# Kernel optimization log

Measured on AMD Instinct MI355X. Metric: run time of the kernel, lower is better.

The kernel has to match this reference:

```python
import jax, jax.numpy as jnp
import numpy as np

N = 100000      # nodes
IN = 64         # in_channels
HID = 64        # hidden_channels
H2 = HID // 2   # per-sign channels
E = 1600000     # edges per sign


def _mean_aggr(x_src, edge_index, num_nodes):
    """Mean of x_src[src] scattered onto dst (PyG mean aggregation)."""
    src, dst = edge_index[0], edge_index[1]
    s = jax.ops.segment_sum(x_src[src], dst, num_segments=num_nodes)
    cnt = jax.ops.segment_sum(jnp.ones((src.shape[0],), x_src.dtype), dst,
                              num_segments=num_nodes)
    return s / jnp.maximum(cnt, 1.0)[:, None]


def setup_inputs() -> dict:
    key = jax.random.key(0)
    ks = jax.random.split(key, 12)
    x = jax.random.normal(ks[0], (N, IN), jnp.float32)
    pos_edge_index = jax.random.randint(ks[1], (2, E), 0, N)
    neg_edge_index = jax.random.randint(ks[2], (2, E), 0, N)

    def w(k, fan_in, fan_out):
        b = 1.0 / np.sqrt(fan_in)
        return jax.random.uniform(k, (fan_in, fan_out), jnp.float32, -b, b)

    return dict(
        x=x, pos_edge_index=pos_edge_index, neg_edge_index=neg_edge_index,
        # conv1 (first_aggr=True): lin_l (no bias applied via l), lin_r (bias)
        w1_pl=w(ks[3], IN, H2), w1_pr=w(ks[4], IN, H2), b1_p=jnp.zeros((H2,), jnp.float32),
        w1_nl=w(ks[5], IN, H2), w1_nr=w(ks[6], IN, H2), b1_n=jnp.zeros((H2,), jnp.float32),
        # conv2 (first_aggr=False): lin_l over cat of two aggregations (2*H2), lin_r over H2
        w2_pl=w(ks[7], 2 * H2, H2), w2_pr=w(ks[8], H2, H2), b2_p=jnp.zeros((H2,), jnp.float32),
        w2_nl=w(ks[9], 2 * H2, H2), w2_nr=w(ks[10], H2, H2), b2_n=jnp.zeros((H2,), jnp.float32),
    )


def reference(x, pos_edge_index, neg_edge_index,
              w1_pl, w1_pr, b1_p, w1_nl, w1_nr, b1_n,
              w2_pl, w2_pr, b2_p, w2_nl, w2_nr, b2_n):
    n = x.shape[0]
    # --- conv1, first_aggr=True ---
    agg_p = _mean_aggr(x, pos_edge_index, n)          # [N, IN]
    agg_n = _mean_aggr(x, neg_edge_index, n)
    out_pos = agg_p @ w1_pl + x @ w1_pr + b1_p         # [N, H2]
    out_neg = agg_n @ w1_nl + x @ w1_nr + b1_n
    z = jax.nn.relu(jnp.concatenate([out_pos, out_neg], axis=-1))  # [N, HID]

    # --- conv2, first_aggr=False ---
    h2 = z.shape[-1] // 2
    zp, zn = z[:, :h2], z[:, h2:]
    p1 = _mean_aggr(zp, pos_edge_index, n)
    p2 = _mean_aggr(zn, neg_edge_index, n)
    out_pos = jnp.concatenate([p1, p2], axis=-1) @ w2_pl + zp @ w2_pr + b2_p
    n1 = _mean_aggr(zn, pos_edge_index, n)
    n2 = _mean_aggr(zp, neg_edge_index, n)
    out_neg = jnp.concatenate([n1, n2], axis=-1) @ w2_nl + zn @ w2_nr + b2_n
    z = jax.nn.relu(jnp.concatenate([out_pos, out_neg], axis=-1))  # [N, HID]
    return z
```

## Files before the change

kernel.cpp:

```cpp
#include <hip/hip_runtime.h>
#include <hip/hip_fp16.h>

using uint = unsigned int;

static constexpr int NN  = 100000;
static constexpr int NE  = 1600000;
static constexpr int DIM = 64;
static constexpr int HH  = 32;
static constexpr int NBLK = (NN + 255) / 256;
static constexpr int HB   = 256;
static constexpr int CHUNK = NE / HB;
static constexpr int BSH  = 9;
static constexpr int BSZ  = 512;
static constexpr int NBKT = (NN + BSZ - 1) / BSZ;

__device__ __forceinline__ float2 up16(uint v) {
  __half2 h = *reinterpret_cast<__half2*>(&v);
  return __half22float2(h);
}
__device__ __forceinline__ uint pk16(float a, float b) {
  __half2 h = __floats2half2_rn(a, b);
  return *reinterpret_cast<uint*>(&h);
}


__global__ void c_hist(const int* __restrict__ pe, const int* __restrict__ ne,
                       int* __restrict__ part_hist) {
  const int set = blockIdx.y;
  const int* dstA = (set ? ne : pe) + NE;
  __shared__ int h[256];
  h[threadIdx.x] = 0;
  __syncthreads();
  int lo = blockIdx.x * CHUNK;
  int hi = lo + CHUNK;
  for (int i = lo + threadIdx.x; i < hi; i += 256)
    atomicAdd(&h[dstA[i] >> BSH], 1);
  __syncthreads();
  part_hist[(set * HB + blockIdx.x) * 256 + threadIdx.x] = h[threadIdx.x];
}

__global__ void c_colscan(int* __restrict__ part_hist, int* __restrict__ tot) {
  const int set = blockIdx.y;
  const int k   = blockIdx.x;
  const int t   = threadIdx.x;
  int v = part_hist[(set * HB + t) * 256 + k];
  __shared__ int sm[256];
  sm[t] = v;
  __syncthreads();
  for (int off = 1; off < 256; off <<= 1) {
    int add = (t >= off) ? sm[t - off] : 0;
    __syncthreads();
    sm[t] += add;
    __syncthreads();
  }
  part_hist[(set * HB + t) * 256 + k] = (t == 0) ? 0 : sm[t - 1];
  if (t == 255) tot[set * 256 + k] = sm[255];
}

__global__ void c_basescan(const int* __restrict__ tot, int* __restrict__ base) {
  const int t   = threadIdx.x;
  const int seg = t >> 8;
  const int idx = t & 255;
  int v = tot[seg * 256 + idx];
  __shared__ int sm[512];
  sm[t] = v;
  __syncthreads();
  for (int off = 1; off < 256; off <<= 1) {
    int add = (idx >= off) ? sm[t - off] : 0;
    __syncthreads();
    sm[t] += add;
    __syncthreads();
  }
  base[seg * 257 + idx] = (idx == 0) ? 0 : sm[t - 1];
  if (idx == 255) base[seg * 257 + 256] = sm[t];
}

__global__ void c_scatter(const int* __restrict__ pe, const int* __restrict__ ne,
                          const int* __restrict__ part_hist, const int* __restrict__ base,
                          int2* __restrict__ partP, int2* __restrict__ partN) {
  const int set = blockIdx.y;
  const int* srcA = set ? ne : pe;
  const int* dstA = srcA + NE;
  int2* part = set ? partN : partP;
  __shared__ int off[256];
  off[threadIdx.x] = base[set * 257 + threadIdx.x] +
                     part_hist[(set * HB + blockIdx.x) * 256 + threadIdx.x];
  __syncthreads();
  int lo = blockIdx.x * CHUNK;
  int hi = lo + CHUNK;
  for (int i = lo + threadIdx.x; i < hi; i += 256) {
    int src = srcA[i];
    int dst = dstA[i];
    int pos = atomicAdd(&off[dst >> BSH], 1);
    part[pos] = make_int2(src, dst);
  }
}

__global__ void c_bucket(const int2* __restrict__ partP, const int2* __restrict__ partN,
                         const int* __restrict__ base,
                         int* __restrict__ row_p, int* __restrict__ row_n,
                         int* __restrict__ col_p, int* __restrict__ col_n,
                         const float* __restrict__ x,
                         const float* __restrict__ w1_pl, const float* __restrict__ w1_pr,
                         const float* __restrict__ b1_p,
                         const float* __restrict__ w1_nl, const float* __restrict__ w1_nr,
                         const float* __restrict__ b1_n,
                         uint* __restrict__ y1u, float* __restrict__ r1) {
  const int bx = blockIdx.x;
  const int t  = threadIdx.x;

  if (bx < 2 * NBKT) {
    const int set = bx / NBKT;
    const int k   = bx - set * NBKT;
    const int2* part = set ? partN : partP;
    int* row = set ? row_n : row_p;
    int* col = set ? col_n : col_p;
    const int lo = k * BSZ;
    const int hi = min(lo + BSZ, NN);
    const int s = base[set * 257 + k];
    const int e = base[set * 257 + k + 1];

    __shared__ int cnt[BSZ], rowl[BSZ], cnt2[BSZ];
    cnt[t] = 0; cnt[t + 256] = 0;
    cnt2[t] = 0; cnt2[t + 256] = 0;
    __syncthreads();
    for (int i = s + t; i < e; i += 256)
      atomicAdd(&cnt[part[i].y - lo], 1);
    __syncthreads();
    rowl[t] = cnt[t]; rowl[t + 256] = cnt[t + 256];
    __syncthreads();
    for (int off = 1; off < BSZ; off <<= 1) {
      int a0 = (t >= off) ? rowl[t - off] : 0;
      int a1 = (t + 256 >= off) ? rowl[t + 256 - off] : 0;
      __syncthreads();
      rowl[t] += a0; rowl[t + 256] += a1;
      __syncthreads();
    }
    if (lo + t < hi)        row[lo + t]        = s + (t ? rowl[t - 1] : 0);
    if (lo + t + 256 < hi)  row[lo + t + 256]  = s + rowl[t + 255];
    if (k == NBKT - 1 && t == 0) row[NN] = NE;
    for (int i = s + t; i < e; i += 256) {
      int2 p = part[i];
      int l = p.y - lo;
      int pos = s + (l ? rowl[l - 1] : 0) + atomicAdd(&cnt2[l], 1);
      col[pos] = p.x;
    }
    return;
  }

  const int pb   = bx - 2 * NBKT;
  const int h    = (pb >= NBLK) ? 1 : 0;
  const int nblk = pb - (h ? NBLK : 0);
  const float* wl   = h ? w1_nl : w1_pl;
  const float* wr   = h ? w1_nr : w1_pr;
  const float* bias = h ? b1_n  : b1_p;

  __shared__ float s_wl[DIM][HH];
  __shared__ float s_wr[DIM][HH];
  for (int i = t; i < DIM * HH; i += 256) {
    s_wl[i >> 5][i & 31] = wl[i];
    s_wr[i >> 5][i & 31] = wr[i];
  }
  __syncthreads();

  int node = nblk * 256 + t;
  if (node >= NN) return;

  float ay[HH], ar[HH];
#pragma unroll
  for (int j = 0; j < HH; ++j) { ay[j] = 0.f; ar[j] = bias[j]; }

  const float4* xrow = (const float4*)(x + (size_t)node * DIM);
#pragma unroll 4
  for (int k4 = 0; k4 < DIM / 4; ++k4) {
    float4 xv = xrow[k4];
#pragma unroll
    for (int u = 0; u < 4; ++u) {
      int k = k4 * 4 + u;
      float xk = (&xv.x)[u];
#pragma unroll
      for (int j = 0; j < HH; ++j) {
        ay[j] += xk * s_wl[k][j];
        ar[j] += xk * s_wr[k][j];
      }
    }
  }

  uint*  yo = y1u + (size_t)node * 32 + h * 16;
  float* ro = r1  + (size_t)node * 64 + h * 32;
#pragma unroll
  for (int j = 0; j < 16; ++j) yo[j] = pk16(ay[2 * j], ay[2 * j + 1]);
#pragma unroll
  for (int j = 0; j < HH; ++j) ro[j] = ar[j];
}

__global__ void k_aggr1(const uint* __restrict__ y1u,
                        const int* __restrict__ rp, const int* __restrict__ cp,
                        const int* __restrict__ rn, const int* __restrict__ cn,
                        const float* r1,
                        float* z) {
  int gid  = blockIdx.x * 256 + threadIdx.x;
  int node = gid >> 6;
  if (node >= NN) return;
  int lane = threadIdx.x & 63;
  int g = lane >> 3;
  int f = lane & 7;

  int s = rp[node], e = rp[node + 1];
  float a0 = 0.f, a1 = 0.f, a2 = 0.f, a3 = 0.f;
  for (int i = s + g; i < e; i += 8) {
    int c = cp[i];
    uint2 v = *(const uint2*)&y1u[(size_t)c * 32 + 2 * f];
    float2 lo = up16(v.x), hi = up16(v.y);
    a0 += lo.x; a1 += lo.y; a2 += hi.x; a3 += hi.y;
  }
#pragma unroll
  for (int w = 8; w <= 32; w <<= 1) {
    a0 += __shfl_xor(a0, w); a1 += __shfl_xor(a1, w);
    a2 += __shfl_xor(a2, w); a3 += __shfl_xor(a3, w);
  }
  float invp = 1.f / (float)max(e - s, 1);

  s = rn[node]; e = rn[node + 1];
  float b0 = 0.f, b1 = 0.f, b2 = 0.f, b3 = 0.f;
  for (int i = s + g; i < e; i += 8) {
    int c = cn[i];
    uint2 v = *(const uint2*)&y1u[(size_t)c * 32 + 16 + 2 * f];
    float2 lo = up16(v.x), hi = up16(v.y);
    b0 += lo.x; b1 += lo.y; b2 += hi.x; b3 += hi.y;
  }
#pragma unroll
  for (int w = 8; w <= 32; w <<= 1) {
    b0 += __shfl_xor(b0, w); b1 += __shfl_xor(b1, w);
    b2 += __shfl_xor(b2, w); b3 += __shfl_xor(b3, w);
  }
  float invn = 1.f / (float)max(e - s, 1);

  size_t base = (size_t)node * 64;
  if (g == 0) {
    const float4 r = *(const float4*)(r1 + base + 4 * f);
    float4 o;
    o.x = fmaxf(a0 * invp + r.x, 0.f);
    o.y = fmaxf(a1 * invp + r.y, 0.f);
    o.z = fmaxf(a2 * invp + r.z, 0.f);
    o.w = fmaxf(a3 * invp + r.w, 0.f);
    *(float4*)(z + base + 4 * f) = o;
  } else if (g == 1) {
    const float4 r = *(const float4*)(r1 + base + 32 + 4 * f);
    float4 o;
    o.x = fmaxf(b0 * invn + r.x, 0.f);
    o.y = fmaxf(b1 * invn + r.y, 0.f);
    o.z = fmaxf(b2 * invn + r.z, 0.f);
    o.w = fmaxf(b3 * invn + r.w, 0.f);
    *(float4*)(z + base + 32 + 4 * f) = o;
  }
}

__global__ void k_mid(const float* __restrict__ z,
                      const float* __restrict__ w2_pl, const float* __restrict__ w2_pr,
                      const float* __restrict__ b2_p,
                      const float* __restrict__ w2_nl, const float* __restrict__ w2_nr,
                      const float* __restrict__ b2_n,
                      uint* __restrict__ u_pos, uint* __restrict__ u_neg,
                      float* __restrict__ r2) {
  const int t = blockIdx.y;
  const float* mat;
  const float* bias = nullptr;
  int srcHalf;
  switch (t) {
    case 0: mat = w2_pl;            srcHalf = 0; break;
    case 1: mat = w2_nl;            srcHalf = 1; break;
    case 2: mat = w2_pl + 32 * 32;  srcHalf = 1; break;
    case 3: mat = w2_nl + 32 * 32;  srcHalf = 0; break;
    case 4: mat = w2_pr; bias = b2_p; srcHalf = 0; break;
    default: mat = w2_nr; bias = b2_n; srcHalf = 1; break;
  }

  __shared__ float s_m[HH][HH];
  for (int i = threadIdx.x; i < HH * HH; i += 256) s_m[i >> 5][i & 31] = mat[i];
  __syncthreads();

  int node = blockIdx.x * 256 + threadIdx.x;
  if (node >= NN) return;

  float acc[HH];
#pragma unroll
  for (int j = 0; j < HH; ++j) acc[j] = bias ? bias[j] : 0.f;

  const float4* zrow = (const float4*)(z + (size_t)node * 64 + srcHalf * 32);
#pragma unroll 4
  for (int k4 = 0; k4 < HH / 4; ++k4) {
    float4 v = zrow[k4];
#pragma unroll
    for (int u = 0; u < 4; ++u) {
      int k = k4 * 4 + u;
      float vv = (&v.x)[u];
#pragma unroll
      for (int j = 0; j < HH; ++j) acc[j] += vv * s_m[k][j];
    }
  }

  if (t < 4) {
    uint* o = (t < 2 ? u_pos : u_neg) + (size_t)node * 32 + (t & 1) * 16;
#pragma unroll
    for (int j = 0; j < 16; ++j) o[j] = pk16(acc[2 * j], acc[2 * j + 1]);
  } else {
    float* o = r2 + (size_t)node * 64 + (t - 4) * 32;
#pragma unroll
    for (int j = 0; j < HH; ++j) o[j] = acc[j];
  }
}

__global__ void k_aggr2(const uint* __restrict__ u_pos, const uint* __restrict__ u_neg,
                        const int* __restrict__ rp, const int* __restrict__ cp,
                        const int* __restrict__ rn, const int* __restrict__ cn,
                        const float* __restrict__ r2,
                        float* __restrict__ out) {
  int gid  = blockIdx.x * 256 + threadIdx.x;
  int node = gid >> 6;
  if (node >= NN) return;
  int lane = threadIdx.x & 63;
  int g = lane >> 4;
  int f = lane & 15;

  int s = rp[node], e = rp[node + 1];
  float a0 = 0.f, a1 = 0.f, a2 = 0.f, a3 = 0.f;
  for (int i = s + g; i < e; i += 4) {
    int c = cp[i];
    uint2 v = *(const uint2*)&u_pos[(size_t)c * 32 + 2 * f];
    float2 lo = up16(v.x), hi = up16(v.y);
    a0 += lo.x; a1 += lo.y; a2 += hi.x; a3 += hi.y;
  }
#pragma unroll
  for (int w = 16; w <= 32; w <<= 1) {
    a0 += __shfl_xor(a0, w); a1 += __shfl_xor(a1, w);
    a2 += __shfl_xor(a2, w); a3 += __shfl_xor(a3, w);
  }
  float invp = 1.f / (float)max(e - s, 1);

  s = rn[node]; e = rn[node + 1];
  float b0 = 0.f, b1 = 0.f, b2 = 0.f, b3 = 0.f;
  for (int i = s + g; i < e; i += 4) {
    int c = cn[i];
    uint2 v = *(const uint2*)&u_neg[(size_t)c * 32 + 2 * f];
    float2 lo = up16(v.x), hi = up16(v.y);
    b0 += lo.x; b1 += lo.y; b2 += hi.x; b3 += hi.y;
  }
#pragma unroll
  for (int w = 16; w <= 32; w <<= 1) {
    b0 += __shfl_xor(b0, w); b1 += __shfl_xor(b1, w);
    b2 += __shfl_xor(b2, w); b3 += __shfl_xor(b3, w);
  }
  float invn = 1.f / (float)max(e - s, 1);

  if (g == 0) {
    size_t base = (size_t)node * 64 + 4 * f;
    const float4 r = *(const float4*)(r2 + base);
    float4 o;
    o.x = fmaxf(a0 * invp + b0 * invn + r.x, 0.f);
    o.y = fmaxf(a1 * invp + b1 * invn + r.y, 0.f);
    o.z = fmaxf(a2 * invp + b2 * invn + r.z, 0.f);
    o.w = fmaxf(a3 * invp + b3 * invn + r.w, 0.f);
    *(float4*)(out + base) = o;
  }
}


extern "C" void kernel_launch(void* const* d_in, const int* in_sizes, int n_in,
                              void* d_out, int out_size, void* d_ws, size_t ws_size,
                              hipStream_t stream) {
  const float* x     = (const float*)d_in[0];
  const int*   pe    = (const int*)d_in[1];
  const int*   ne    = (const int*)d_in[2];
  const float* w1_pl = (const float*)d_in[3];
  const float* w1_pr = (const float*)d_in[4];
  const float* b1_p  = (const float*)d_in[5];
  const float* w1_nl = (const float*)d_in[6];
  const float* w1_nr = (const float*)d_in[7];
  const float* b1_n  = (const float*)d_in[8];
  const float* w2_pl = (const float*)d_in[9];
  const float* w2_pr = (const float*)d_in[10];
  const float* b2_p  = (const float*)d_in[11];
  const float* w2_nl = (const float*)d_in[12];
  const float* w2_nr = (const float*)d_in[13];
  const float* b2_n  = (const float*)d_in[14];

  char* ws = (char*)d_ws;
  size_t off = 0;
  auto alloc = [&](size_t bytes) -> char* {
    char* p = ws + off;
    off = (off + bytes + 255) & ~(size_t)255;
    return p;
  };

  int* row_p = (int*)alloc((size_t)(NN + 1) * 4);
  int* row_n = (int*)alloc((size_t)(NN + 1) * 4);
  int* col_p = (int*)alloc((size_t)NE * 4);
  int* col_n = (int*)alloc((size_t)NE * 4);
  int* part_hist = (int*)alloc((size_t)2 * HB * 256 * 4);
  int* tot   = (int*)alloc((size_t)2 * 256 * 4);
  int* base  = (int*)alloc((size_t)2 * 257 * 4);

  char* regA  = alloc((size_t)2 * NE * 8);
  int2* partP = (int2*)regA;
  int2* partN = (int2*)(regA + (size_t)NE * 8);
  uint* u_pos = (uint*)regA;
  uint* u_neg = (uint*)(regA + (size_t)NN * 32 * 4);

  char*  regB = alloc((size_t)NN * 64 * 4);
  uint*  y1u  = (uint*)regB;
  float* r2   = (float*)regB;

  float* r1 = (float*)d_out;
  float* z  = (float*)d_out;

  const int nb = NBLK;
  const int ab = (NN * 64 + 255) / 256;

  dim3 hg(HB, 2);
  c_hist<<<hg, 256, 0, stream>>>(pe, ne, part_hist);
  dim3 cg(256, 2);
  c_colscan<<<cg, 256, 0, stream>>>(part_hist, tot);
  c_basescan<<<1, 512, 0, stream>>>(tot, base);
  c_scatter<<<hg, 256, 0, stream>>>(pe, ne, part_hist, base, partP, partN);
  c_bucket<<<2 * NBKT + 2 * NBLK, 256, 0, stream>>>(
      partP, partN, base, row_p, row_n, col_p, col_n,
      x, w1_pl, w1_pr, b1_p, w1_nl, w1_nr, b1_n, y1u, r1);

  k_aggr1<<<ab, 256, 0, stream>>>(y1u, row_p, col_p, row_n, col_n, r1, z);

  dim3 g2(nb, 6);
  k_mid<<<g2, 256, 0, stream>>>(z, w2_pl, w2_pr, b2_p, w2_nl, w2_nr, b2_n,
                                u_pos, u_neg, r2);

  k_aggr2<<<ab, 256, 0, stream>>>(u_pos, u_neg, row_p, col_p, row_n, col_n, r2,
                                  (float*)d_out);
}
```

Baseline: 318.5 us.

## Pack partition entries into one word and widen gather loads to 16 bytes

The partition buffer now stores each edge as a single 32-bit word, with the source shifted left and the bucket-local destination in the low 9 bits, replacing the int2 pair. This halves scatter and bucket-pass traffic and shrinks the workspace region. Both aggregation kernels now load 16 bytes per lane (8 halves) with more edge groups per node, which adds shuffle-reduction steps in exchange for fewer, wider gather loads. Packing relies on source indices fitting in 23 bits, which holds for the 100000 nodes.

```diff
diff --git a/kernel.cpp b/kernel.cpp
--- a/kernel.cpp
+++ b/kernel.cpp
@@ -77,11 +77,11 @@
 
 __global__ void c_scatter(const int* __restrict__ pe, const int* __restrict__ ne,
                           const int* __restrict__ part_hist, const int* __restrict__ base,
-                          int2* __restrict__ partP, int2* __restrict__ partN) {
+                          uint* __restrict__ partP, uint* __restrict__ partN) {
   const int set = blockIdx.y;
   const int* srcA = set ? ne : pe;
   const int* dstA = srcA + NE;
-  int2* part = set ? partN : partP;
+  uint* part = set ? partN : partP;
   __shared__ int off[256];
   off[threadIdx.x] = base[set * 257 + threadIdx.x] +
                      part_hist[(set * HB + blockIdx.x) * 256 + threadIdx.x];
@@ -92,11 +92,11 @@
     int src = srcA[i];
     int dst = dstA[i];
     int pos = atomicAdd(&off[dst >> BSH], 1);
-    part[pos] = make_int2(src, dst);
-  }
-}
-
-__global__ void c_bucket(const int2* __restrict__ partP, const int2* __restrict__ partN,
+    part[pos] = ((uint)src << BSH) | (uint)(dst & (BSZ - 1));
+  }
+}
+
+__global__ void c_bucket(const uint* __restrict__ partP, const uint* __restrict__ partN,
                          const int* __restrict__ base,
                          int* __restrict__ row_p, int* __restrict__ row_n,
                          int* __restrict__ col_p, int* __restrict__ col_n,
@@ -112,7 +112,7 @@
   if (bx < 2 * NBKT) {
     const int set = bx / NBKT;
     const int k   = bx - set * NBKT;
-    const int2* part = set ? partN : partP;
+    const uint* part = set ? partN : partP;
     int* row = set ? row_n : row_p;
     int* col = set ? col_n : col_p;
     const int lo = k * BSZ;
@@ -125,7 +125,7 @@
     cnt2[t] = 0; cnt2[t + 256] = 0;
     __syncthreads();
     for (int i = s + t; i < e; i += 256)
-      atomicAdd(&cnt[part[i].y - lo], 1);
+      atomicAdd(&cnt[part[i] & (BSZ - 1)], 1);
     __syncthreads();
     rowl[t] = cnt[t]; rowl[t + 256] = cnt[t + 256];
     __syncthreads();
@@ -140,10 +140,10 @@
     if (lo + t + 256 < hi)  row[lo + t + 256]  = s + rowl[t + 255];
     if (k == NBKT - 1 && t == 0) row[NN] = NE;
     for (int i = s + t; i < e; i += 256) {
-      int2 p = part[i];
-      int l = p.y - lo;
+      uint p = part[i];
+      int l = p & (BSZ - 1);
       int pos = s + (l ? rowl[l - 1] : 0) + atomicAdd(&cnt2[l], 1);
-      col[pos] = p.x;
+      col[pos] = (int)(p >> BSH);
     }
     return;
   }
@@ -203,56 +203,74 @@
   int node = gid >> 6;
   if (node >= NN) return;
   int lane = threadIdx.x & 63;
-  int g = lane >> 3;
-  int f = lane & 7;
+  int g = lane >> 2;
+  int f = lane & 3;
 
   int s = rp[node], e = rp[node + 1];
-  float a0 = 0.f, a1 = 0.f, a2 = 0.f, a3 = 0.f;
-  for (int i = s + g; i < e; i += 8) {
+  float a[8];
+#pragma unroll
+  for (int j = 0; j < 8; ++j) a[j] = 0.f;
+  for (int i = s + g; i < e; i += 16) {
     int c = cp[i];
-    uint2 v = *(const uint2*)&y1u[(size_t)c * 32 + 2 * f];
-    float2 lo = up16(v.x), hi = up16(v.y);
-    a0 += lo.x; a1 += lo.y; a2 += hi.x; a3 += hi.y;
-  }
-#pragma unroll
-  for (int w = 8; w <= 32; w <<= 1) {
-    a0 += __shfl_xor(a0, w); a1 += __shfl_xor(a1, w);
-    a2 += __shfl_xor(a2, w); a3 += __shfl_xor(a3, w);
+    uint4 v = *(const uint4*)&y1u[(size_t)c * 32 + 4 * f];
+    float2 p0 = up16(v.x), p1 = up16(v.y), p2 = up16(v.z), p3 = up16(v.w);
+    a[0] += p0.x; a[1] += p0.y; a[2] += p1.x; a[3] += p1.y;
+    a[4] += p2.x; a[5] += p2.y; a[6] += p3.x; a[7] += p3.y;
+  }
+#pragma unroll
+  for (int w = 4; w <= 32; w <<= 1) {
+#pragma unroll
+    for (int j = 0; j < 8; ++j) a[j] += __shfl_xor(a[j], w);
   }
   float invp = 1.f / (float)max(e - s, 1);
 
   s = rn[node]; e = rn[node + 1];
-  float b0 = 0.f, b1 = 0.f, b2 = 0.f, b3 = 0.f;
-  for (int i = s + g; i < e; i += 8) {
+  float b[8];
+#pragma unroll
+  for (int j = 0; j < 8; ++j) b[j] = 0.f;
+  for (int i = s + g; i < e; i += 16) {
     int c = cn[i];
-    uint2 v = *(const uint2*)&y1u[(size_t)c * 32 + 16 + 2 * f];
-    float2 lo = up16(v.x), hi = up16(v.y);
-    b0 += lo.x; b1 += lo.y; b2 += hi.x; b3 += hi.y;
-  }
-#pragma unroll
-  for (int w = 8; w <= 32; w <<= 1) {
-    b0 += __shfl_xor(b0, w); b1 += __shfl_xor(b1, w);
-    b2 += __shfl_xor(b2, w); b3 += __shfl_xor(b3, w);
+    uint4 v = *(const uint4*)&y1u[(size_t)c * 32 + 16 + 4 * f];
+    float2 p0 = up16(v.x), p1 = up16(v.y), p2 = up16(v.z), p3 = up16(v.w);
+    b[0] += p0.x; b[1] += p0.y; b[2] += p1.x; b[3] += p1.y;
+    b[4] += p2.x; b[5] += p2.y; b[6] += p3.x; b[7] += p3.y;
+  }
+#pragma unroll
+  for (int w = 4; w <= 32; w <<= 1) {
+#pragma unroll
+    for (int j = 0; j < 8; ++j) b[j] += __shfl_xor(b[j], w);
   }
   float invn = 1.f / (float)max(e - s, 1);
 
   size_t base = (size_t)node * 64;
   if (g == 0) {
-    const float4 r = *(const float4*)(r1 + base + 4 * f);
-    float4 o;
-    o.x = fmaxf(a0 * invp + r.x, 0.f);
-    o.y = fmaxf(a1 * invp + r.y, 0.f);
-    o.z = fmaxf(a2 * invp + r.z, 0.f);
-    o.w = fmaxf(a3 * invp + r.w, 0.f);
-    *(float4*)(z + base + 4 * f) = o;
+    const float4 r0 = *(const float4*)(r1 + base + 8 * f);
+    const float4 r1v = *(const float4*)(r1 + base + 8 * f + 4);
+    float4 o0, o1;
+    o0.x = fmaxf(a[0] * invp + r0.x, 0.f);
+    o0.y = fmaxf(a[1] * invp + r0.y, 0.f);
+    o0.z = fmaxf(a[2] * invp + r0.z, 0.f);
+    o0.w = fmaxf(a[3] * invp + r0.w, 0.f);
+    o1.x = fmaxf(a[4] * invp + r1v.x, 0.f);
+    o1.y = fmaxf(a[5] * invp + r1v.y, 0.f);
+    o1.z = fmaxf(a[6] * invp + r1v.z, 0.f);
+    o1.w = fmaxf(a[7] * invp + r1v.w, 0.f);
+    *(float4*)(z + base + 8 * f) = o0;
+    *(float4*)(z + base + 8 * f + 4) = o1;
   } else if (g == 1) {
-    const float4 r = *(const float4*)(r1 + base + 32 + 4 * f);
-    float4 o;
-    o.x = fmaxf(b0 * invn + r.x, 0.f);
-    o.y = fmaxf(b1 * invn + r.y, 0.f);
-    o.z = fmaxf(b2 * invn + r.z, 0.f);
-    o.w = fmaxf(b3 * invn + r.w, 0.f);
-    *(float4*)(z + base + 32 + 4 * f) = o;
+    const float4 r0 = *(const float4*)(r1 + base + 32 + 8 * f);
+    const float4 r1v = *(const float4*)(r1 + base + 32 + 8 * f + 4);
+    float4 o0, o1;
+    o0.x = fmaxf(b[0] * invn + r0.x, 0.f);
+    o0.y = fmaxf(b[1] * invn + r0.y, 0.f);
+    o0.z = fmaxf(b[2] * invn + r0.z, 0.f);
+    o0.w = fmaxf(b[3] * invn + r0.w, 0.f);
+    o1.x = fmaxf(b[4] * invn + r1v.x, 0.f);
+    o1.y = fmaxf(b[5] * invn + r1v.y, 0.f);
+    o1.z = fmaxf(b[6] * invn + r1v.z, 0.f);
+    o1.w = fmaxf(b[7] * invn + r1v.w, 0.f);
+    *(float4*)(z + base + 32 + 8 * f) = o0;
+    *(float4*)(z + base + 32 + 8 * f + 4) = o1;
   }
 }
 
@@ -320,48 +338,60 @@
   int node = gid >> 6;
   if (node >= NN) return;
   int lane = threadIdx.x & 63;
-  int g = lane >> 4;
-  int f = lane & 15;
+  int g = lane >> 3;
+  int f = lane & 7;
 
   int s = rp[node], e = rp[node + 1];
-  float a0 = 0.f, a1 = 0.f, a2 = 0.f, a3 = 0.f;
-  for (int i = s + g; i < e; i += 4) {
+  float a[8];
+#pragma unroll
+  for (int j = 0; j < 8; ++j) a[j] = 0.f;
+  for (int i = s + g; i < e; i += 8) {
     int c = cp[i];
-    uint2 v = *(const uint2*)&u_pos[(size_t)c * 32 + 2 * f];
-    float2 lo = up16(v.x), hi = up16(v.y);
-    a0 += lo.x; a1 += lo.y; a2 += hi.x; a3 += hi.y;
-  }
-#pragma unroll
-  for (int w = 16; w <= 32; w <<= 1) {
-    a0 += __shfl_xor(a0, w); a1 += __shfl_xor(a1, w);
-    a2 += __shfl_xor(a2, w); a3 += __shfl_xor(a3, w);
+    uint4 v = *(const uint4*)&u_pos[(size_t)c * 32 + 4 * f];
+    float2 p0 = up16(v.x), p1 = up16(v.y), p2 = up16(v.z), p3 = up16(v.w);
+    a[0] += p0.x; a[1] += p0.y; a[2] += p1.x; a[3] += p1.y;
+    a[4] += p2.x; a[5] += p2.y; a[6] += p3.x; a[7] += p3.y;
+  }
+#pragma unroll
+  for (int w = 8; w <= 32; w <<= 1) {
+#pragma unroll
+    for (int j = 0; j < 8; ++j) a[j] += __shfl_xor(a[j], w);
   }
   float invp = 1.f / (float)max(e - s, 1);
 
   s = rn[node]; e = rn[node + 1];
-  float b0 = 0.f, b1 = 0.f, b2 = 0.f, b3 = 0.f;
-  for (int i = s + g; i < e; i += 4) {
+  float b[8];
+#pragma unroll
+  for (int j = 0; j < 8; ++j) b[j] = 0.f;
+  for (int i = s + g; i < e; i += 8) {
     int c = cn[i];
-    uint2 v = *(const uint2*)&u_neg[(size_t)c * 32 + 2 * f];
-    float2 lo = up16(v.x), hi = up16(v.y);
-    b0 += lo.x; b1 += lo.y; b2 += hi.x; b3 += hi.y;
-  }
-#pragma unroll
-  for (int w = 16; w <= 32; w <<= 1) {
-    b0 += __shfl_xor(b0, w); b1 += __shfl_xor(b1, w);
-    b2 += __shfl_xor(b2, w); b3 += __shfl_xor(b3, w);
+    uint4 v = *(const uint4*)&u_neg[(size_t)c * 32 + 4 * f];
+    float2 p0 = up16(v.x), p1 = up16(v.y), p2 = up16(v.z), p3 = up16(v.w);
+    b[0] += p0.x; b[1] += p0.y; b[2] += p1.x; b[3] += p1.y;
+    b[4] += p2.x; b[5] += p2.y; b[6] += p3.x; b[7] += p3.y;
+  }
+#pragma unroll
+  for (int w = 8; w <= 32; w <<= 1) {
+#pragma unroll
+    for (int j = 0; j < 8; ++j) b[j] += __shfl_xor(b[j], w);
   }
   float invn = 1.f / (float)max(e - s, 1);
 
   if (g == 0) {
-    size_t base = (size_t)node * 64 + 4 * f;
-    const float4 r = *(const float4*)(r2 + base);
-    float4 o;
-    o.x = fmaxf(a0 * invp + b0 * invn + r.x, 0.f);
-    o.y = fmaxf(a1 * invp + b1 * invn + r.y, 0.f);
-    o.z = fmaxf(a2 * invp + b2 * invn + r.z, 0.f);
-    o.w = fmaxf(a3 * invp + b3 * invn + r.w, 0.f);
-    *(float4*)(out + base) = o;
+    size_t base = (size_t)node * 64 + 8 * f;
+    const float4 r0 = *(const float4*)(r2 + base);
+    const float4 r1v = *(const float4*)(r2 + base + 4);
+    float4 o0, o1;
+    o0.x = fmaxf(a[0] * invp + b[0] * invn + r0.x, 0.f);
+    o0.y = fmaxf(a[1] * invp + b[1] * invn + r0.y, 0.f);
+    o0.z = fmaxf(a[2] * invp + b[2] * invn + r0.z, 0.f);
+    o0.w = fmaxf(a[3] * invp + b[3] * invn + r0.w, 0.f);
+    o1.x = fmaxf(a[4] * invp + b[4] * invn + r1v.x, 0.f);
+    o1.y = fmaxf(a[5] * invp + b[5] * invn + r1v.y, 0.f);
+    o1.z = fmaxf(a[6] * invp + b[6] * invn + r1v.z, 0.f);
+    o1.w = fmaxf(a[7] * invp + b[7] * invn + r1v.w, 0.f);
+    *(float4*)(out + base) = o0;
+    *(float4*)(out + base + 4) = o1;
   }
 }
 
@@ -401,9 +431,9 @@
   int* tot   = (int*)alloc((size_t)2 * 256 * 4);
   int* base  = (int*)alloc((size_t)2 * 257 * 4);
 
-  char* regA  = alloc((size_t)2 * NE * 8);
-  int2* partP = (int2*)regA;
-  int2* partN = (int2*)(regA + (size_t)NE * 8);
+  char* regA  = alloc((size_t)NN * 64 * 4);
+  uint* partP = (uint*)regA;
+  uint* partN = (uint*)(regA + (size_t)NE * 4);
   uint* u_pos = (uint*)regA;
   uint* u_neg = (uint*)(regA + (size_t)NN * 32 * 4);
 
```

Result: faster. 287.3 us (-9.8%).
